# Kernel optimization log

Hardware: AMD Instinct MI355X
Metric: run time of the kernel (lower is better)

The kernel has to match this reference:

```python
import jax, jax.numpy as jnp
import numpy as np

N_USERS = 6144
N_ITEMS = 12288
N_NODES = N_USERS + N_ITEMS
D = 64
AVG_DEG = 32
NNZ = N_NODES * AVG_DEG
N_LAYERS = 2
K = 30  # module keeps top (k+1) per row


def setup_inputs() -> dict:
    key = jax.random.key(0)
    k1, k2, k3, k4, k5 = jax.random.split(key, 5)
    user_emb = 0.1 * jax.random.normal(k1, (N_USERS, D), dtype=jnp.float32)
    item_emb = 0.1 * jax.random.normal(k2, (N_ITEMS, D), dtype=jnp.float32)
    edge_row = jax.random.randint(k3, (NNZ,), 0, N_NODES, dtype=jnp.int32)
    edge_col = jax.random.randint(k4, (NNZ,), 0, N_NODES, dtype=jnp.int32)
    # normalized-adjacency-like values (positive, ~1/deg scale)
    edge_val = jax.random.uniform(k5, (NNZ,), dtype=jnp.float32) / AVG_DEG
    return {
        "user_emb": user_emb,
        "item_emb": item_emb,
        "edge_row": edge_row,
        "edge_col": edge_col,
        "edge_val": edge_val,
    }


def _spmm(edge_row, edge_col, edge_val, x):
    # y[r] = sum_{(r,c) in E} val * x[c]   -- torch.sparse.mm equivalent (COO)
    return jax.ops.segment_sum(edge_val[:, None] * x[edge_col], edge_row,
                               num_segments=N_NODES)


def reference(user_emb, item_emb, edge_row, edge_col, edge_val):
    # LightGCN propagation
    all_emb = jnp.concatenate([user_emb, item_emb], axis=0)  # [N, D]
    embs = [all_emb]
    for _ in range(N_LAYERS):
        all_emb = _spmm(edge_row, edge_col, edge_val, all_emb)
        embs.append(all_emb)
    light_out = jnp.mean(jnp.stack(embs, axis=1), axis=1)  # [N, D]

    items = light_out[N_USERS:]  # [N_ITEMS, D]
    # F.normalize(dim=1, p=2) with eps clamp
    norm = jnp.linalg.norm(items, axis=1, keepdims=True)
    items = items / jnp.maximum(norm, 1e-12)

    # dense pairwise similarity
    sim = items @ items.T  # [N_ITEMS, N_ITEMS]

    # top_k: keep top (k+1) values per row, zero elsewhere
    vals, idx = jax.lax.top_k(sim, K + 1)  # [N_ITEMS, K+1]
    rows = jnp.arange(sim.shape[0])[:, None]
    sparse_sim = jnp.zeros_like(sim).at[rows, idx].set(vals)

    # apply_non_linearity('relu', i) -> relu
    return jax.nn.relu(sparse_sim)
```

## Files before the change

### kernel.cpp

```cpp
#include <hip/hip_runtime.h>
#include <hip/hip_bf16.h>

#define N_USERS 6144
#define N_ITEMS 12288
#define N_NODES 18432
#define D 64
#define NNZ 589824
#define K_TOP 31
#define NCAND_MIN 48
#define NCAND_MAX 240
#define CMAX 256

using frag_ab = __attribute__((ext_vector_type(8))) short;
using frag_cd = __attribute__((ext_vector_type(4))) float;
using uint4_e = __attribute__((ext_vector_type(4))) unsigned;
using uint2_e = __attribute__((ext_vector_type(2))) unsigned;
using float4_e = __attribute__((ext_vector_type(4))) float;

__device__ inline unsigned f32_to_bf16_bits(float f) {
    unsigned b = __float_as_uint(f);
    return (b + 0x7FFFu + ((b >> 16) & 1u)) >> 16;
}

__global__ void concat64_kernel(const float* __restrict__ u,
                                const float* __restrict__ it,
                                double* __restrict__ e0) {
    int i = blockIdx.x * 256 + threadIdx.x;
    const int NU = N_USERS * D;
    e0[i] = (i < NU) ? (double)u[i] : (double)it[i - NU];
}

__global__ void count_kernel(const int* __restrict__ er, int* __restrict__ cnt) {
    int e = blockIdx.x * 256 + threadIdx.x;
    atomicAdd(&cnt[er[e]], 1);
}

__global__ __launch_bounds__(256) void scan_kernel(const int* __restrict__ cnt,
                                                   int* __restrict__ row_start,
                                                   int* __restrict__ cursor) {
    __shared__ int part[256];
    int t = threadIdx.x;
    const int PER = N_NODES / 256;
    int s = 0;
    for (int i = 0; i < PER; ++i) s += cnt[t * PER + i];
    part[t] = s;
    __syncthreads();
    for (int off = 1; off < 256; off <<= 1) {
        int v = part[t];
        int w = (t >= off) ? part[t - off] : 0;
        __syncthreads();
        part[t] = v + w;
        __syncthreads();
    }
    int run = (t == 0) ? 0 : part[t - 1];
    for (int i = 0; i < PER; ++i) {
        int idx = t * PER + i;
        row_start[idx] = run;
        cursor[idx] = run;
        run += cnt[idx];
    }
    if (t == 255) row_start[N_NODES] = run;
}

__global__ void scatter_kernel(const int* __restrict__ er, const int* __restrict__ ec,
                               const float* __restrict__ ev,
                               int* __restrict__ cursor, int2* __restrict__ ep) {
    int e = blockIdx.x * 256 + threadIdx.x;
    int r = er[e];
    int pos = atomicAdd(&cursor[r], 1);
    ep[pos] = make_int2(ec[e], __float_as_int(ev[e]));
}

__global__ __launch_bounds__(256) void spmm_csr_kernel(const int* __restrict__ row_start,
                                                       const int2* __restrict__ ep,
                                                       const double* __restrict__ x,
                                                       double* __restrict__ y) {
    int t = threadIdx.x;
    int lane = t & 63, wave = t >> 6;
    int row = blockIdx.x * 4 + wave;
    if (row >= N_NODES) return;
    int beg = row_start[row], end = row_start[row + 1];
    double a0 = 0.0, a1 = 0.0, a2 = 0.0, a3 = 0.0;
    int j = beg;
    int n4 = beg + ((end - beg) & ~3);
    for (; j < n4; j += 4) {
        int2 p0 = ep[j], p1 = ep[j + 1], p2 = ep[j + 2], p3 = ep[j + 3];
        a0 += (double)__int_as_float(p0.y) * x[(size_t)p0.x * D + lane];
        a1 += (double)__int_as_float(p1.y) * x[(size_t)p1.x * D + lane];
        a2 += (double)__int_as_float(p2.y) * x[(size_t)p2.x * D + lane];
        a3 += (double)__int_as_float(p3.y) * x[(size_t)p3.x * D + lane];
    }
    for (; j < end; ++j) {
        int2 p = ep[j];
        a0 += (double)__int_as_float(p.y) * x[(size_t)p.x * D + lane];
    }
    y[(size_t)row * D + lane] = (a0 + a1) + (a2 + a3);
}

__global__ void mean_norm64_kernel(const double* __restrict__ e0,
                                   const double* __restrict__ e1,
                                   const double* __restrict__ e2,
                                   double* __restrict__ xn64,
                                   ushort* __restrict__ xh) {
    int t = threadIdx.x;
    int wave = t >> 6, lane = t & 63;
    int r = blockIdx.x * 4 + wave;
    size_t g = (size_t)(r + N_USERS) * D + lane;
    double s = (e0[g] + e1[g] + e2[g]) / 3.0;
    double ss = s * s;
    #pragma unroll
    for (int off = 32; off; off >>= 1) ss += __shfl_xor(ss, off);
    double norm = sqrt(ss);
    double denom = fmax(norm, 1e-12);
    double v = s / denom;
    xn64[(size_t)r * D + lane] = v;
    xh[(size_t)r * D + lane] = (ushort)f32_to_bf16_bits((float)v);
}

#define LDS_STRIDE 72
#define OST_STRIDE 132
__global__ __launch_bounds__(256) void simgemm_kernel(const ushort* __restrict__ Xh,
                                                      ushort* __restrict__ Cb) {
    __shared__ __align__(16) ushort S[2 * 128 * LDS_STRIDE];
    ushort* Als = S;
    ushort* Bls = S + 128 * LDS_STRIDE;
    int t = threadIdx.x;
    int bi = blockIdx.y, bj = blockIdx.x;

    #pragma unroll
    for (int p = 0; p < 4; ++p) {
        int u4 = t + 256 * p;
        int row = u4 >> 3;
        int seg = u4 & 7;
        *(uint4_e*)&Als[row * LDS_STRIDE + seg * 8] =
            *(const uint4_e*)&Xh[(size_t)(bi * 128 + row) * D + seg * 8];
        *(uint4_e*)&Bls[row * LDS_STRIDE + seg * 8] =
            *(const uint4_e*)&Xh[(size_t)(bj * 128 + row) * D + seg * 8];
    }
    __syncthreads();

    int lane = t & 63, wave = t >> 6;
    int wrow = (wave >> 1) * 64, wcol = (wave & 1) * 64;
    int ml = lane & 15, quad = lane >> 4;

    frag_cd acc[4][4] = {};
    #pragma unroll
    for (int s = 0; s < 2; ++s) {
        frag_ab af[4], bf[4];
        int koff = s * 32 + quad * 8;
        #pragma unroll
        for (int rt = 0; rt < 4; ++rt)
            af[rt] = *(const frag_ab*)&Als[(wrow + rt * 16 + ml) * LDS_STRIDE + koff];
        #pragma unroll
        for (int ct = 0; ct < 4; ++ct)
            bf[ct] = *(const frag_ab*)&Bls[(wcol + ct * 16 + ml) * LDS_STRIDE + koff];
        #pragma unroll
        for (int rt = 0; rt < 4; ++rt)
            #pragma unroll
            for (int ct = 0; ct < 4; ++ct)
                acc[rt][ct] = __builtin_amdgcn_mfma_f32_16x16x32_bf16(
                    af[rt], bf[ct], acc[rt][ct], 0, 0, 0);
    }
    __syncthreads();

    ushort* Ost = S;
    #pragma unroll
    for (int rt = 0; rt < 4; ++rt) {
        #pragma unroll
        for (int ct = 0; ct < 4; ++ct) {
            int row = wrow + rt * 16 + quad * 4;
            int col = wcol + ct * 16 + ml;
            #pragma unroll
            for (int r = 0; r < 4; ++r)
                Ost[(row + r) * OST_STRIDE + col] = (ushort)f32_to_bf16_bits(acc[rt][ct][r]);
        }
    }
    __syncthreads();

    const size_t base = (size_t)(bi * 128) * N_ITEMS + bj * 128;
    #pragma unroll
    for (int p = 0; p < 16; ++p) {
        int i = t + 256 * p;
        int row = i >> 5, cp = i & 31;
        uint2_e v = *(const uint2_e*)&Ost[row * OST_STRIDE + cp * 4];
        __builtin_nontemporal_store(v, (uint2_e*)(Cb + base + (size_t)row * N_ITEMS + cp * 4));
    }
}

__global__ __launch_bounds__(256) void topk_kernel(const ushort* __restrict__ Cb,
                                                   float* __restrict__ Cout,
                                                   const double* __restrict__ xn64) {
    __shared__ int s_red[4];
    __shared__ unsigned s_cnt;
    __shared__ int    candi[CMAX];
    __shared__ double candv[CMAX];
    __shared__ double s_xr[D];
    int t = threadIdx.x;
    int r = blockIdx.x;
    const uint4_e* Crow4 = (const uint4_e*)(Cb + (size_t)r * N_ITEMS);

    unsigned short u[48];
    #pragma unroll
    for (int j = 0; j < 6; ++j) {
        uint4_e f = __builtin_nontemporal_load(&Crow4[t + 256 * j]);
        #pragma unroll
        for (int q = 0; q < 4; ++q) {
            unsigned w = f[q];
            unsigned lo = w & 0xFFFFu, hi = w >> 16;
            u[j * 8 + 2 * q]     = (unsigned short)(lo ^ ((lo & 0x8000u) ? 0xFFFFu : 0x8000u));
            u[j * 8 + 2 * q + 1] = (unsigned short)(hi ^ ((hi & 0x8000u) ? 0xFFFFu : 0x8000u));
        }
    }
    if (t < D) s_xr[t] = xn64[(size_t)r * D + t];

    unsigned lo = 0u, hi = 0xFFFFu, T = 0u, bestT = 0u;
    int found = 0;
    for (int it = 0; it < 16; ++it) {
        unsigned mid = lo + ((hi - lo) >> 1);
        int c = 0;
        #pragma unroll
        for (int k = 0; k < 48; ++k) c += (u[k] >= mid) ? 1 : 0;
        #pragma unroll
        for (int off = 32; off; off >>= 1) c += __shfl_down(c, off);
        if ((t & 63) == 0) s_red[t >> 6] = c;
        __syncthreads();
        int ctot = s_red[0] + s_red[1] + s_red[2] + s_red[3];
        __syncthreads();
        if (ctot >= NCAND_MIN) {
            bestT = mid;
            if (ctot <= NCAND_MAX) { T = mid; found = 1; }
            else lo = mid + 1;
        } else {
            if (mid == 0u) { found = 1; T = bestT; }
            else hi = mid - 1;
        }
        if (found || lo > hi) break;
    }
    if (!found) T = bestT;

    if (t == 0) s_cnt = 0;
    __syncthreads();
    #pragma unroll
    for (int k = 0; k < 48; ++k) {
        if (u[k] >= (unsigned short)T) {
            unsigned pos = atomicAdd(&s_cnt, 1u);
            if (pos < CMAX) candi[pos] = 8 * (t + 256 * (k >> 3)) + (k & 7);
        }
    }
    __syncthreads();
    int c = (int)s_cnt; if (c > CMAX) c = CMAX;

    if (t < c) {
        const double* xc = xn64 + (size_t)candi[t] * D;
        double acc = 0.0;
        #pragma unroll 8
        for (int k = 0; k < D; ++k) acc += s_xr[k] * xc[k];
        candv[t] = acc;
    }
    __syncthreads();

    int   sel_idx = -1;
    float sel_val = 0.f;
    if (t < c) {
        double v = candv[t];
        int    id = candi[t];
        int rank = 0;
        for (int j = 0; j < c; ++j) {
            double vj = candv[j];
            rank += (vj > v || (vj == v && candi[j] < id)) ? 1 : 0;
        }
        if (rank < K_TOP) {
            sel_idx = id;
            sel_val = (v > 0.0) ? (float)v : 0.f;
        }
    }

    float4_e* Orow4 = (float4_e*)(Cout + (size_t)r * N_ITEMS);
    float4_e z = {0.f, 0.f, 0.f, 0.f};
    #pragma unroll
    for (int j = 0; j < 12; ++j)
        __builtin_nontemporal_store(z, &Orow4[t + 256 * j]);
    __syncthreads();
    if (sel_idx >= 0) Cout[(size_t)r * N_ITEMS + sel_idx] = sel_val;
}

extern "C" void kernel_launch(void* const* d_in, const int* in_sizes, int n_in,
                              void* d_out, int out_size, void* d_ws, size_t ws_size,
                              hipStream_t stream) {
    const float* user_emb = (const float*)d_in[0];
    const float* item_emb = (const float*)d_in[1];
    const int*   edge_row = (const int*)d_in[2];
    const int*   edge_col = (const int*)d_in[3];
    const float* edge_val = (const float*)d_in[4];
    float* C = (float*)d_out;

    double* e0d  = (double*)d_ws;
    double* e1d  = e0d + (size_t)N_NODES * D;
    double* e2d  = e1d + (size_t)N_NODES * D;
    double* xn64 = e2d + (size_t)N_NODES * D;
    int2*   ep   = (int2*)(xn64 + (size_t)N_ITEMS * D);
    ushort* xh   = (ushort*)(ep + NNZ);
    ushort* Cb   = xh + (size_t)N_ITEMS * D;
    int*  cnt       = (int*)(Cb + (size_t)N_ITEMS * N_ITEMS);
    int*  row_start = cnt + N_NODES;
    int*  cursor    = row_start + N_NODES + 1;

    (void)hipMemsetAsync(cnt, 0, N_NODES * sizeof(int), stream);

    concat64_kernel<<<N_NODES * D / 256, 256, 0, stream>>>(user_emb, item_emb, e0d);

    count_kernel<<<NNZ / 256, 256, 0, stream>>>(edge_row, cnt);
    scan_kernel<<<1, 256, 0, stream>>>(cnt, row_start, cursor);
    scatter_kernel<<<NNZ / 256, 256, 0, stream>>>(edge_row, edge_col, edge_val, cursor, ep);

    spmm_csr_kernel<<<(N_NODES + 3) / 4, 256, 0, stream>>>(row_start, ep, e0d, e1d);
    spmm_csr_kernel<<<(N_NODES + 3) / 4, 256, 0, stream>>>(row_start, ep, e1d, e2d);

    mean_norm64_kernel<<<N_ITEMS / 4, 256, 0, stream>>>(e0d, e1d, e2d, xn64, xh);

    dim3 ggrid(N_ITEMS / 128, N_ITEMS / 128);
    simgemm_kernel<<<ggrid, 256, 0, stream>>>(xh, Cb);

    topk_kernel<<<N_ITEMS, 256, 0, stream>>>(Cb, C, xn64);
}
```

Before: 960.5 us.

## Quantize similarity matrix to u8, simplify threshold search, parallelize CSR scan

The intermediate similarity matrix is stored as 8-bit quantized values instead of bf16, halving the write traffic in the GEMM and the read traffic in the top-k kernel. The top-k threshold search becomes a fixed 8-step binary search over 256 levels with a larger minimum candidate count, and candidates are then re-scored exactly in fp64. The single-block scan is split into three multi-block kernels. Coarse 8-bit quantization risks many ties, which could overflow the 256-candidate buffer and drop true top-k entries.

```diff
diff --git a/kernel.cpp b/kernel.cpp
--- a/kernel.cpp
+++ b/kernel.cpp
@@ -7,8 +7,7 @@
 #define D 64
 #define NNZ 589824
 #define K_TOP 31
-#define NCAND_MIN 48
-#define NCAND_MAX 240
+#define NCAND_MIN 96
 #define CMAX 256
 
 using frag_ab = __attribute__((ext_vector_type(8))) short;
@@ -20,6 +19,11 @@
 __device__ inline unsigned f32_to_bf16_bits(float f) {
     unsigned b = __float_as_uint(f);
     return (b + 0x7FFFu + ((b >> 16) & 1u)) >> 16;
+}
+__device__ inline unsigned char sim_to_u8(float v) {
+    float e = rintf(fmaf(v, 127.5f, 127.5f));
+    e = fminf(fmaxf(e, 0.f), 255.f);
+    return (unsigned char)(int)e;
 }
 
 __global__ void concat64_kernel(const float* __restrict__ u,
@@ -35,31 +39,53 @@
     atomicAdd(&cnt[er[e]], 1);
 }
 
-__global__ __launch_bounds__(256) void scan_kernel(const int* __restrict__ cnt,
-                                                   int* __restrict__ row_start,
-                                                   int* __restrict__ cursor) {
-    __shared__ int part[256];
-    int t = threadIdx.x;
-    const int PER = N_NODES / 256;
-    int s = 0;
-    for (int i = 0; i < PER; ++i) s += cnt[t * PER + i];
-    part[t] = s;
+__global__ __launch_bounds__(256) void scanA_kernel(const int* __restrict__ cnt,
+                                                    int* __restrict__ excl,
+                                                    int* __restrict__ bsum) {
+    __shared__ int sh[256];
+    int t = threadIdx.x, b = blockIdx.x;
+    int idx = b * 256 + t;
+    int v = cnt[idx];
+    sh[t] = v;
     __syncthreads();
     for (int off = 1; off < 256; off <<= 1) {
-        int v = part[t];
-        int w = (t >= off) ? part[t - off] : 0;
-        __syncthreads();
-        part[t] = v + w;
-        __syncthreads();
-    }
-    int run = (t == 0) ? 0 : part[t - 1];
-    for (int i = 0; i < PER; ++i) {
-        int idx = t * PER + i;
-        row_start[idx] = run;
-        cursor[idx] = run;
-        run += cnt[idx];
-    }
-    if (t == 255) row_start[N_NODES] = run;
+        int x = sh[t];
+        int y = (t >= off) ? sh[t - off] : 0;
+        __syncthreads();
+        sh[t] = x + y;
+        __syncthreads();
+    }
+    excl[idx] = sh[t] - v;
+    if (t == 255) bsum[b] = sh[255];
+}
+
+__global__ __launch_bounds__(128) void scanB_kernel(const int* __restrict__ bsum,
+                                                    int* __restrict__ bpre) {
+    __shared__ int sh[128];
+    int t = threadIdx.x;
+    const int NB = N_NODES / 256;
+    int v = (t < NB) ? bsum[t] : 0;
+    sh[t] = v;
+    __syncthreads();
+    for (int off = 1; off < 128; off <<= 1) {
+        int x = sh[t];
+        int y = (t >= off) ? sh[t - off] : 0;
+        __syncthreads();
+        sh[t] = x + y;
+        __syncthreads();
+    }
+    if (t < NB) bpre[t] = sh[t] - v;
+}
+
+__global__ __launch_bounds__(256) void scanC_kernel(const int* __restrict__ excl,
+                                                    const int* __restrict__ bpre,
+                                                    int* __restrict__ row_start,
+                                                    int* __restrict__ cursor) {
+    int idx = blockIdx.x * 256 + threadIdx.x;
+    int v = excl[idx] + bpre[idx >> 8];
+    row_start[idx] = v;
+    cursor[idx] = v;
+    if (idx == 0) row_start[N_NODES] = NNZ;
 }
 
 __global__ void scatter_kernel(const int* __restrict__ er, const int* __restrict__ ec,
@@ -118,9 +144,9 @@
 }
 
 #define LDS_STRIDE 72
-#define OST_STRIDE 132
+#define OST_STRIDE 136
 __global__ __launch_bounds__(256) void simgemm_kernel(const ushort* __restrict__ Xh,
-                                                      ushort* __restrict__ Cb) {
+                                                      unsigned char* __restrict__ Cu8) {
     __shared__ __align__(16) ushort S[2 * 128 * LDS_STRIDE];
     ushort* Als = S;
     ushort* Bls = S + 128 * LDS_STRIDE;
@@ -163,7 +189,7 @@
     }
     __syncthreads();
 
-    ushort* Ost = S;
+    unsigned char* Ost = (unsigned char*)S;
     #pragma unroll
     for (int rt = 0; rt < 4; ++rt) {
         #pragma unroll
@@ -172,22 +198,22 @@
             int col = wcol + ct * 16 + ml;
             #pragma unroll
             for (int r = 0; r < 4; ++r)
-                Ost[(row + r) * OST_STRIDE + col] = (ushort)f32_to_bf16_bits(acc[rt][ct][r]);
+                Ost[(row + r) * OST_STRIDE + col] = sim_to_u8(acc[rt][ct][r]);
         }
     }
     __syncthreads();
 
     const size_t base = (size_t)(bi * 128) * N_ITEMS + bj * 128;
     #pragma unroll
-    for (int p = 0; p < 16; ++p) {
+    for (int p = 0; p < 8; ++p) {
         int i = t + 256 * p;
-        int row = i >> 5, cp = i & 31;
-        uint2_e v = *(const uint2_e*)&Ost[row * OST_STRIDE + cp * 4];
-        __builtin_nontemporal_store(v, (uint2_e*)(Cb + base + (size_t)row * N_ITEMS + cp * 4));
-    }
-}
-
-__global__ __launch_bounds__(256) void topk_kernel(const ushort* __restrict__ Cb,
+        int row = i >> 4, seg = i & 15;
+        uint2_e v = *(const uint2_e*)&Ost[row * OST_STRIDE + seg * 8];
+        __builtin_nontemporal_store(v, (uint2_e*)(Cu8 + base + (size_t)row * N_ITEMS + seg * 8));
+    }
+}
+
+__global__ __launch_bounds__(256) void topk_kernel(const unsigned char* __restrict__ Cu8,
                                                    float* __restrict__ Cout,
                                                    const double* __restrict__ xn64) {
     __shared__ int s_red[4];
@@ -197,54 +223,47 @@
     __shared__ double s_xr[D];
     int t = threadIdx.x;
     int r = blockIdx.x;
-    const uint4_e* Crow4 = (const uint4_e*)(Cb + (size_t)r * N_ITEMS);
-
-    unsigned short u[48];
-    #pragma unroll
-    for (int j = 0; j < 6; ++j) {
+    const uint4_e* Crow4 = (const uint4_e*)(Cu8 + (size_t)r * N_ITEMS);
+
+    unsigned char u[48];
+    #pragma unroll
+    for (int j = 0; j < 3; ++j) {
         uint4_e f = __builtin_nontemporal_load(&Crow4[t + 256 * j]);
         #pragma unroll
         for (int q = 0; q < 4; ++q) {
             unsigned w = f[q];
-            unsigned lo = w & 0xFFFFu, hi = w >> 16;
-            u[j * 8 + 2 * q]     = (unsigned short)(lo ^ ((lo & 0x8000u) ? 0xFFFFu : 0x8000u));
-            u[j * 8 + 2 * q + 1] = (unsigned short)(hi ^ ((hi & 0x8000u) ? 0xFFFFu : 0x8000u));
+            u[j * 16 + q * 4 + 0] = (unsigned char)(w & 0xFF);
+            u[j * 16 + q * 4 + 1] = (unsigned char)((w >> 8) & 0xFF);
+            u[j * 16 + q * 4 + 2] = (unsigned char)((w >> 16) & 0xFF);
+            u[j * 16 + q * 4 + 3] = (unsigned char)(w >> 24);
         }
     }
     if (t < D) s_xr[t] = xn64[(size_t)r * D + t];
 
-    unsigned lo = 0u, hi = 0xFFFFu, T = 0u, bestT = 0u;
-    int found = 0;
-    for (int it = 0; it < 16; ++it) {
-        unsigned mid = lo + ((hi - lo) >> 1);
+    int lo = 0, hi = 255;
+    #pragma unroll
+    for (int it = 0; it < 8; ++it) {
+        int mid = (lo + hi + 1) >> 1;
         int c = 0;
         #pragma unroll
-        for (int k = 0; k < 48; ++k) c += (u[k] >= mid) ? 1 : 0;
+        for (int k = 0; k < 48; ++k) c += ((int)u[k] >= mid) ? 1 : 0;
         #pragma unroll
         for (int off = 32; off; off >>= 1) c += __shfl_down(c, off);
         if ((t & 63) == 0) s_red[t >> 6] = c;
         __syncthreads();
         int ctot = s_red[0] + s_red[1] + s_red[2] + s_red[3];
         __syncthreads();
-        if (ctot >= NCAND_MIN) {
-            bestT = mid;
-            if (ctot <= NCAND_MAX) { T = mid; found = 1; }
-            else lo = mid + 1;
-        } else {
-            if (mid == 0u) { found = 1; T = bestT; }
-            else hi = mid - 1;
-        }
-        if (found || lo > hi) break;
-    }
-    if (!found) T = bestT;
+        if (ctot >= NCAND_MIN) lo = mid; else hi = mid - 1;
+    }
+    int T = lo;
 
     if (t == 0) s_cnt = 0;
     __syncthreads();
     #pragma unroll
     for (int k = 0; k < 48; ++k) {
-        if (u[k] >= (unsigned short)T) {
+        if ((int)u[k] >= T) {
             unsigned pos = atomicAdd(&s_cnt, 1u);
-            if (pos < CMAX) candi[pos] = 8 * (t + 256 * (k >> 3)) + (k & 7);
+            if (pos < CMAX) candi[pos] = 16 * (t + 256 * (k >> 4)) + (k & 15);
         }
     }
     __syncthreads();
@@ -300,17 +319,22 @@
     double* xn64 = e2d + (size_t)N_NODES * D;
     int2*   ep   = (int2*)(xn64 + (size_t)N_ITEMS * D);
     ushort* xh   = (ushort*)(ep + NNZ);
-    ushort* Cb   = xh + (size_t)N_ITEMS * D;
-    int*  cnt       = (int*)(Cb + (size_t)N_ITEMS * N_ITEMS);
-    int*  row_start = cnt + N_NODES;
+    unsigned char* Cu8 = (unsigned char*)(xh + (size_t)N_ITEMS * D);
+    int*  cnt       = (int*)(Cu8 + (size_t)N_ITEMS * N_ITEMS);
+    int*  excl      = cnt + N_NODES;
+    int*  row_start = excl + N_NODES;
     int*  cursor    = row_start + N_NODES + 1;
+    int*  bsum      = cursor + N_NODES;
+    int*  bpre      = bsum + 128;
 
     (void)hipMemsetAsync(cnt, 0, N_NODES * sizeof(int), stream);
 
     concat64_kernel<<<N_NODES * D / 256, 256, 0, stream>>>(user_emb, item_emb, e0d);
 
     count_kernel<<<NNZ / 256, 256, 0, stream>>>(edge_row, cnt);
-    scan_kernel<<<1, 256, 0, stream>>>(cnt, row_start, cursor);
+    scanA_kernel<<<N_NODES / 256, 256, 0, stream>>>(cnt, excl, bsum);
+    scanB_kernel<<<1, 128, 0, stream>>>(bsum, bpre);
+    scanC_kernel<<<N_NODES / 256, 256, 0, stream>>>(excl, bpre, row_start, cursor);
     scatter_kernel<<<NNZ / 256, 256, 0, stream>>>(edge_row, edge_col, edge_val, cursor, ep);
 
     spmm_csr_kernel<<<(N_NODES + 3) / 4, 256, 0, stream>>>(row_start, ep, e0d, e1d);
@@ -319,7 +343,7 @@
     mean_norm64_kernel<<<N_ITEMS / 4, 256, 0, stream>>>(e0d, e1d, e2d, xn64, xh);
 
     dim3 ggrid(N_ITEMS / 128, N_ITEMS / 128);
-    simgemm_kernel<<<ggrid, 256, 0, stream>>>(xh, Cb);
-
-    topk_kernel<<<N_ITEMS, 256, 0, stream>>>(Cb, C, xn64);
-}
+    simgemm_kernel<<<ggrid, 256, 0, stream>>>(xh, Cu8);
+
+    topk_kernel<<<N_ITEMS, 256, 0, stream>>>(Cu8, C, xn64);
+}
```

Result: faster. 922.8 us (-3.9%).
